# Performance work log

Hardware: AMD Instinct MI355X
Metric: run time of the kernel (lower is better)

The kernel has to match this reference:

```python
import jax, jax.numpy as jnp
import numpy as np

HIDDEN = 2048
NUM_HEADS = 16
HEAD_DIM = 128
INNER = NUM_HEADS * HEAD_DIM
ROPE_BASE = 10000.0


def apply_rope(x):
    # x: [B, H, S, D], rotate-half (NeoX-style) RoPE
    B, H, S, D = x.shape
    inv_freq = 1.0 / (ROPE_BASE ** (jnp.arange(0, D, 2, dtype=jnp.float32) / D))
    t = jnp.arange(S, dtype=jnp.float32)
    freqs = t[:, None] * inv_freq[None, :]          # [S, D/2]
    cos = jnp.concatenate([jnp.cos(freqs)] * 2, -1)  # [S, D]
    sin = jnp.concatenate([jnp.sin(freqs)] * 2, -1)
    x1, x2 = x[..., : D // 2], x[..., D // 2:]
    rotated = jnp.concatenate([-x2, x1], axis=-1)
    return x * cos[None, None] + rotated * sin[None, None]


def setup_inputs() -> dict:
    key = jax.random.key(0)
    ks = jax.random.split(key, 9)
    s = 1.0 / np.sqrt(HIDDEN)
    return {
        "hidden_states": jax.random.normal(ks[0], (2, 2048, HIDDEN), jnp.float32),
        "Wq": jax.random.uniform(ks[1], (INNER, HIDDEN), jnp.float32, -s, s),
        "bq": jax.random.uniform(ks[2], (INNER,), jnp.float32, -s, s),
        "Wk": jax.random.uniform(ks[3], (INNER, HIDDEN), jnp.float32, -s, s),
        "bk": jax.random.uniform(ks[4], (INNER,), jnp.float32, -s, s),
        "Wv": jax.random.uniform(ks[5], (INNER, HIDDEN), jnp.float32, -s, s),
        "bv": jax.random.uniform(ks[6], (INNER,), jnp.float32, -s, s),
        "Wo": jax.random.uniform(ks[7], (HIDDEN, INNER), jnp.float32, -s, s),
        "bo": jax.random.uniform(ks[8], (HIDDEN,), jnp.float32, -s, s),
    }


def reference(hidden_states, Wq, bq, Wk, bk, Wv, bv, Wo, bo):
    B, S, _ = hidden_states.shape

    def heads(x):  # [B,S,inner] -> [B,H,S,D]
        return x.reshape(B, S, NUM_HEADS, HEAD_DIM).transpose(0, 2, 1, 3)

    q = heads(hidden_states @ Wq.T + bq)
    k = heads(hidden_states @ Wk.T + bk)
    v = heads(hidden_states @ Wv.T + bv)
    q = apply_rope(q)
    k = apply_rope(k)

    scores = jnp.einsum("bhqd,bhkd->bhqk", q, k) / jnp.sqrt(
        jnp.asarray(HEAD_DIM, q.dtype))
    causal = jnp.tril(jnp.ones((S, S), dtype=bool))
    scores = jnp.where(causal[None, None], scores, jnp.finfo(scores.dtype).min)
    weights = jax.nn.softmax(scores, axis=-1)
    context = jnp.einsum("bhqk,bhkd->bhqd", weights, v)
    merged = context.transpose(0, 2, 1, 3).reshape(B, S, INNER)
    return merged @ Wo.T + bo
```

## Files before the change

### kernel.cpp

```cpp
#include <hip/hip_runtime.h>

using u16 = unsigned short;
using u32 = unsigned int;

typedef __attribute__((ext_vector_type(4))) float f32x4;
typedef __attribute__((ext_vector_type(8))) short frag8;

#define HIDDEN 2048
#define SEQ    2048
#define NHEADS 16
#define HDIM   128

__device__ __forceinline__ float bf2f(u16 u) {
  union { u32 i; float f; } c; c.i = ((u32)u) << 16; return c.f;
}
__device__ __forceinline__ u16 f2bf(float f) {
  union { float f; u32 i; } c; c.f = f;
  u32 u = c.i + 0x7fffu + ((c.i >> 16) & 1u);
  return (u16)(u >> 16);
}

__global__ void cvt_all(const float* __restrict__ X,
                        const float* __restrict__ W0, const float* __restrict__ W1,
                        const float* __restrict__ W2, const float* __restrict__ W3,
                        u16* __restrict__ dX,
                        u16* __restrict__ dW0, u16* __restrict__ dW1,
                        u16* __restrict__ dW2, u16* __restrict__ dW3)
{
  const int bx = blockIdx.x;
  const float* s; u16* d; int g;
  if (bx < 4096) { s = X; d = dX; g = bx * 256 + threadIdx.x; }
  else {
    const int t = bx - 4096;
    const int w = t >> 11;
    s = (w == 0) ? W0 : (w == 1) ? W1 : (w == 2) ? W2 : W3;
    d = (w == 0) ? dW0 : (w == 1) ? dW1 : (w == 2) ? dW2 : dW3;
    g = (t & 2047) * 256 + threadIdx.x;
  }
  const float* p = s + (size_t)g * 8;
  f32x4 x0 = *(const f32x4*)p, x1 = *(const f32x4*)(p + 4);
  frag8 o;
#pragma unroll
  for (int e = 0; e < 4; e++) { o[e] = (short)f2bf(x0[e]); o[e+4] = (short)f2bf(x1[e]); }
  *(frag8*)(d + (size_t)g * 8) = o;
}

template<int W_BF16, int NW, int VT, int C_F32>
__global__ __launch_bounds__(256, 4)
void gemm_fused(const u16* __restrict__ A,
                const void* __restrict__ W0, const void* __restrict__ W1,
                const void* __restrict__ W2,
                const float* __restrict__ bias0, const float* __restrict__ bias1,
                const float* __restrict__ bias2,
                void* __restrict__ C0, void* __restrict__ C1, void* __restrict__ C2)
{
  __shared__ __align__(16) u16 smem[8192];
  u16* As = smem;
  u16* Bs = smem + 4096;

  const int tid  = threadIdx.x;
  const int lane = tid & 63;
  const int wv   = tid >> 6;
  const int quad = lane >> 4;
  const int l16  = lane & 15;
  const int wm = wv >> 1, wn = wv & 1;
  const int m0 = blockIdx.y * 128;
  const int wix = (NW == 1) ? 0 : (blockIdx.x >> 4);
  const int n0  = ((NW == 1) ? blockIdx.x : (blockIdx.x & 15)) * 128;

  const void* Wp = (wix == 0) ? W0 : (wix == 1) ? W1 : W2;
  const float* bias = (wix == 0) ? bias0 : (wix == 1) ? bias1 : bias2;
  void* Cp = (wix == 0) ? C0 : (wix == 1) ? C1 : C2;

  f32x4 acc[4][4];
#pragma unroll
  for (int i = 0; i < 4; i++)
#pragma unroll
    for (int j = 0; j < 4; j++) acc[i][j] = (f32x4)0.0f;

  const int g0 = tid, g1 = tid + 256;
  const int r0 = g0 >> 2, c0 = (g0 & 3) * 8;
  const int r1 = g1 >> 2, c1 = (g1 & 3) * 8;

  for (int k0 = 0; k0 < HIDDEN; k0 += 32) {
    __builtin_amdgcn_global_load_lds(
      (const __attribute__((address_space(1))) void*)(A + (size_t)(m0 + r0) * HIDDEN + k0 + c0),
      (__attribute__((address_space(3))) void*)(As + g0 * 8), 16, 0, 0);
    __builtin_amdgcn_global_load_lds(
      (const __attribute__((address_space(1))) void*)(A + (size_t)(m0 + r1) * HIDDEN + k0 + c1),
      (__attribute__((address_space(3))) void*)(As + g1 * 8), 16, 0, 0);
    if (W_BF16) {
      const u16* Wb = (const u16*)Wp;
      __builtin_amdgcn_global_load_lds(
        (const __attribute__((address_space(1))) void*)(Wb + (size_t)(n0 + r0) * HIDDEN + k0 + c0),
        (__attribute__((address_space(3))) void*)(Bs + g0 * 8), 16, 0, 0);
      __builtin_amdgcn_global_load_lds(
        (const __attribute__((address_space(1))) void*)(Wb + (size_t)(n0 + r1) * HIDDEN + k0 + c1),
        (__attribute__((address_space(3))) void*)(Bs + g1 * 8), 16, 0, 0);
    } else {
      const float* Wf = (const float*)Wp;
      const float* p0 = Wf + (size_t)(n0 + r0) * HIDDEN + k0 + c0;
      const float* p1 = Wf + (size_t)(n0 + r1) * HIDDEN + k0 + c1;
      f32x4 x0 = *(const f32x4*)p0, x1 = *(const f32x4*)(p0 + 4);
      f32x4 y0 = *(const f32x4*)p1, y1 = *(const f32x4*)(p1 + 4);
      frag8 b0v, b1v;
#pragma unroll
      for (int e = 0; e < 4; e++) {
        b0v[e]   = (short)f2bf(x0[e]); b0v[e+4] = (short)f2bf(x1[e]);
        b1v[e]   = (short)f2bf(y0[e]); b1v[e+4] = (short)f2bf(y1[e]);
      }
      *(frag8*)&Bs[g0 * 8] = b0v;
      *(frag8*)&Bs[g1 * 8] = b1v;
    }

    __builtin_amdgcn_s_waitcnt(0);
    __syncthreads();

    frag8 af[4], bfr[4];
#pragma unroll
    for (int mt = 0; mt < 4; mt++)
      af[mt] = *(const frag8*)&As[(wm*64 + mt*16 + l16) * 32 + quad*8];
#pragma unroll
    for (int nt = 0; nt < 4; nt++)
      bfr[nt] = *(const frag8*)&Bs[(wn*64 + nt*16 + l16) * 32 + quad*8];
#pragma unroll
    for (int mt = 0; mt < 4; mt++)
#pragma unroll
      for (int nt = 0; nt < 4; nt++)
        acc[mt][nt] = __builtin_amdgcn_mfma_f32_16x16x32_bf16(af[mt], bfr[nt], acc[mt][nt], 0, 0, 0);

    __syncthreads();
  }

  if (VT && wix == 2) {
    u16* Cv = (u16*)Cp;
    u16* T = smem + wv * 1056;
#pragma unroll
    for (int nt = 0; nt < 4; nt++) {
      const int n  = n0 + wn*64 + nt*16 + l16;
      const float bv = bias[n];
#pragma unroll
      for (int mt = 0; mt < 4; mt++)
#pragma unroll
        for (int r = 0; r < 4; r++)
          T[l16 * 66 + mt*16 + quad*4 + r] = f2bf(acc[mt][nt][r] + bv);
#pragma unroll
      for (int rr = 0; rr < 16; rr++) {
        const int nn = n0 + wn*64 + nt*16 + rr;
        const int mm = m0 + wm*64 + lane;
        const int b = mm >> 11, s = mm & 2047;
        Cv[((size_t)(b * HIDDEN + nn)) * SEQ + s] = T[rr * 66 + lane];
      }
    }
  } else {
#pragma unroll
    for (int nt = 0; nt < 4; nt++) {
      const int n  = n0 + wn*64 + nt*16 + l16;
      const float bv = bias[n];
#pragma unroll
      for (int mt = 0; mt < 4; mt++) {
#pragma unroll
        for (int r = 0; r < 4; r++) {
          const int m = m0 + wm*64 + mt*16 + quad*4 + r;
          if (C_F32) ((float*)Cp)[(size_t)m * HIDDEN + n] = acc[mt][nt][r] + bv;
          else       ((u16*)Cp)[(size_t)m * HIDDEN + n]   = f2bf(acc[mt][nt][r] + bv);
        }
      }
    }
  }
}

#define NT32 32

#define STG(gptr, lofs) __builtin_amdgcn_global_load_lds( \
    (const __attribute__((address_space(1))) void*)(gptr), \
    (__attribute__((address_space(3))) void*)(smem + (lofs)), 16, 0, 0)

#define GRP(t, DOSTAGE, WAITSTR) { \
  u16* As = smem + ((t) % 3) * 24576; \
  u16* Bs = As + 16384; \
  frag8 af[8], bfr[2]; \
  _Pragma("unroll") for (int mt = 0; mt < 8; mt++) \
    af[mt] = *(const frag8*)(As + abase + mt*1024 + s0q); \
  bfr[0] = *(const frag8*)(Bs + bbase + s0q); \
  bfr[1] = *(const frag8*)(Bs + bbase + 1024 + s0q); \
  if (DOSTAGE) { \
    const size_t ko = (size_t)((t)+2)*64; const int sb = (((t)+2)%3)*24576; \
    STG(gA0 + ko, sb + ldsA0); STG(gA1 + ko, sb + ldsA1); STG(gB0 + ko, sb + ldsB0); \
  } \
  __builtin_amdgcn_s_barrier(); \
  __builtin_amdgcn_s_setprio(1); \
  _Pragma("unroll") for (int mt = 0; mt < 8; mt++) { \
    acc[mt][0] = __builtin_amdgcn_mfma_f32_16x16x32_bf16(af[mt], bfr[0], acc[mt][0], 0,0,0); \
    acc[mt][1] = __builtin_amdgcn_mfma_f32_16x16x32_bf16(af[mt], bfr[1], acc[mt][1], 0,0,0); \
  } \
  __builtin_amdgcn_s_setprio(0); \
  __builtin_amdgcn_s_barrier(); \
  _Pragma("unroll") for (int mt = 0; mt < 8; mt++) \
    af[mt] = *(const frag8*)(As + abase + mt*1024 + s1q); \
  bfr[0] = *(const frag8*)(Bs + bbase + s1q); \
  bfr[1] = *(const frag8*)(Bs + bbase + 1024 + s1q); \
  if (DOSTAGE) { \
    const size_t ko = (size_t)((t)+2)*64; const int sb = (((t)+2)%3)*24576; \
    STG(gA2 + ko, sb + ldsA2); STG(gA3 + ko, sb + ldsA3); STG(gB1 + ko, sb + ldsB1); \
  } \
  __builtin_amdgcn_s_barrier(); \
  __builtin_amdgcn_s_setprio(1); \
  _Pragma("unroll") for (int mt = 0; mt < 8; mt++) { \
    acc[mt][0] = __builtin_amdgcn_mfma_f32_16x16x32_bf16(af[mt], bfr[0], acc[mt][0], 0,0,0); \
    acc[mt][1] = __builtin_amdgcn_mfma_f32_16x16x32_bf16(af[mt], bfr[1], acc[mt][1], 0,0,0); \
  } \
  __builtin_amdgcn_s_setprio(0); \
  asm volatile("s_waitcnt " WAITSTR ::: "memory"); \
  __builtin_amdgcn_s_barrier(); \
}

#define G256_SETUP(Abase, Wbase) \
  const int tid  = threadIdx.x; \
  const int lane = tid & 63; \
  const int wv   = tid >> 6; \
  const int quad = lane >> 4; \
  const int l16  = lane & 15; \
  const int wm = wv >> 2, wn = wv & 3; \
  const int c8 = (lane & 7) ^ (lane >> 3); \
  const int rA = lane >> 3; \
  const u16* gA0 = (Abase) + (size_t)(m0 + wv*32 +  0 + rA) * HIDDEN + c8*8; \
  const u16* gA1 = (Abase) + (size_t)(m0 + wv*32 +  8 + rA) * HIDDEN + c8*8; \
  const u16* gA2 = (Abase) + (size_t)(m0 + wv*32 + 16 + rA) * HIDDEN + c8*8; \
  const u16* gA3 = (Abase) + (size_t)(m0 + wv*32 + 24 + rA) * HIDDEN + c8*8; \
  const u16* gB0 = (Wbase) + (size_t)(n0 + wv*16 +  0 + rA) * HIDDEN + c8*8; \
  const u16* gB1 = (Wbase) + (size_t)(n0 + wv*16 +  8 + rA) * HIDDEN + c8*8; \
  const int ldsA0 = (4*wv)*512 + lane*8; \
  const int ldsA1 = ldsA0 + 512; \
  const int ldsA2 = ldsA0 + 1024; \
  const int ldsA3 = ldsA0 + 1536; \
  const int ldsB0 = 16384 + (2*wv)*512 + lane*8; \
  const int ldsB1 = ldsB0 + 512; \
  const int s0q = ((quad    ) ^ (l16 & 7)) * 8; \
  const int s1q = ((quad + 4) ^ (l16 & 7)) * 8; \
  const int abase = (wm*128 + l16) * 64; \
  const int bbase = (wn*32  + l16) * 64; \
  f32x4 acc[8][2]; \
  _Pragma("unroll") \
  for (int i = 0; i < 8; i++) { acc[i][0] = (f32x4)0.0f; acc[i][1] = (f32x4)0.0f; } \
  STG(gA0, ldsA0); STG(gA1, ldsA1); STG(gB0, ldsB0); \
  STG(gA2, ldsA2); STG(gA3, ldsA3); STG(gB1, ldsB1); \
  STG(gA0 + 64, 24576 + ldsA0); STG(gA1 + 64, 24576 + ldsA1); STG(gB0 + 64, 24576 + ldsB0); \
  STG(gA2 + 64, 24576 + ldsA2); STG(gA3 + 64, 24576 + ldsA3); STG(gB1 + 64, 24576 + ldsB1); \
  asm volatile("s_waitcnt vmcnt(6)" ::: "memory"); \
  __builtin_amdgcn_s_barrier(); \
  for (int t = 0; t < NT32 - 2; ++t) GRP(t, 1, "vmcnt(6)"); \
  GRP(NT32 - 2, 0, "vmcnt(0)"); \
  GRP(NT32 - 1, 0, "vmcnt(63)");

__global__ __launch_bounds__(512, 2)
void gemm256_qkv(const u16* __restrict__ A,
                 const u16* __restrict__ W0, const u16* __restrict__ W1,
                 const u16* __restrict__ W2,
                 const float* __restrict__ bias0, const float* __restrict__ bias1,
                 const float* __restrict__ bias2,
                 u16* __restrict__ C0, u16* __restrict__ C1, u16* __restrict__ Vt)
{
  __shared__ __align__(16) u16 smem[73728];

  const int bid = blockIdx.x;
  const int sbid = (bid & 7) * 96 + (bid >> 3);
  const int colTile = sbid >> 4;
  const int rowTile = sbid & 15;
  const int wix = colTile >> 4;
  const int n0  = (colTile & 15) * 128;
  const int m0  = rowTile * 256;

  const u16* Wp = (wix == 0) ? W0 : (wix == 1) ? W1 : W2;
  const float* bias = (wix == 0) ? bias0 : (wix == 1) ? bias1 : bias2;

  G256_SETUP(A, Wp)

  if (wix != 2) {
    u16* Cb = (wix == 0) ? C0 : C1;
#pragma unroll
    for (int nt = 0; nt < 2; nt++) {
      const int n = n0 + wn*32 + nt*16 + l16;
      const float bv = bias[n];
#pragma unroll
      for (int mt = 0; mt < 8; mt++) {
        const int m = m0 + wm*128 + mt*16 + quad*4;
#pragma unroll
        for (int r = 0; r < 4; r++)
          Cb[(size_t)(m + r) * HIDDEN + n] = f2bf(acc[mt][nt][r] + bv);
      }
    }
  } else {
    u16* T = smem + wv * 2176;
    const int b  = m0 >> 11;
    const int s0 = (m0 & 2047) + wm*128;
#pragma unroll
    for (int nt = 0; nt < 2; nt++) {
      const int nloc = n0 + wn*32 + nt*16;
      const float bv = bias[nloc + l16];
#pragma unroll
      for (int mt = 0; mt < 8; mt++)
#pragma unroll
        for (int r = 0; r < 4; r++)
          T[l16*136 + mt*16 + quad*4 + r] = f2bf(acc[mt][nt][r] + bv);
#pragma unroll
      for (int rr = 0; rr < 16; rr++) {
        const size_t vb = ((size_t)(b * HIDDEN + nloc + rr)) * SEQ + s0;
        Vt[vb + lane]      = T[rr*136 + lane];
        Vt[vb + 64 + lane] = T[rr*136 + 64 + lane];
      }
    }
  }
}

__global__ __launch_bounds__(512, 2)
void gemm256_o(const u16* __restrict__ A, const u16* __restrict__ W,
               const float* __restrict__ bias, float* __restrict__ C)
{
  __shared__ __align__(16) u16 smem[73728];

  const int bid = blockIdx.x;
  const int sbid = (bid & 7) * 32 + (bid >> 3);
  const int colTile = sbid >> 4;
  const int rowTile = sbid & 15;
  const int n0  = colTile * 128;
  const int m0  = rowTile * 256;

  G256_SETUP(A, W)

#pragma unroll
  for (int nt = 0; nt < 2; nt++) {
    const int n = n0 + wn*32 + nt*16 + l16;
    const float bv = bias[n];
#pragma unroll
    for (int mt = 0; mt < 8; mt++) {
      const int m = m0 + wm*128 + mt*16 + quad*4;
#pragma unroll
      for (int r = 0; r < 4; r++)
        C[(size_t)(m + r) * HIDDEN + n] = acc[mt][nt][r] + bv;
    }
  }
}

__global__ void rope_kernel(u16* __restrict__ Q, u16* __restrict__ K)
{
  const int tid = blockIdx.x * 256 + threadIdx.x;
  const int t   = tid >> 19;
  const int r   = tid & 524287;
  const int row = r >> 7;
  const int grp = r & 127;
  const int h   = grp >> 3, d0 = (grp & 7) * 8;
  u16* X = t ? K : Q;
  const float s = (float)(row & 2047);
  const float qscale = t ? 1.0f : 0.08838834764831845f;
  const size_t base = (size_t)row * HIDDEN + h * HDIM + d0;
  frag8 a = *(const frag8*)(X + base);
  frag8 b = *(const frag8*)(X + base + 64);
  frag8 oa, ob;
#pragma unroll
  for (int e = 0; e < 8; e++) {
    const float inv = __expf(-(float)(d0 + e) * (9.210340371976184f / 64.0f));
    float sn, c;
    __sincosf(s * inv, &sn, &c);
    const float x1 = bf2f((u16)a[e]), x2 = bf2f((u16)b[e]);
    oa[e] = (short)f2bf((x1 * c - x2 * sn) * qscale);
    ob[e] = (short)f2bf((x2 * c + x1 * sn) * qscale);
  }
  *(frag8*)(X + base)      = oa;
  *(frag8*)(X + base + 64) = ob;
}

__global__ __launch_bounds__(256, 4)
void attn_kernel(const u16* Q, const u16* __restrict__ K,
                 const u16* __restrict__ Vt, u16* O)
{
  __shared__ __align__(16) u16 smem[20480];

  const int bx = blockIdx.x;
  const int g  = bx >> 5;
  const int bh = bx & 31;
  const int qt = (g & 1) ? (31 - (g >> 1)) : (g >> 1);
  const int b = bh >> 4, h = bh & 15;

  const int tid = threadIdx.x, lane = tid & 63, wv = tid >> 6;
  const int quad = lane >> 4, l16 = lane & 15;
  const int l7 = l16 & 7;

  const size_t krow0 = (size_t)(b * SEQ) * HIDDEN + h * HDIM;
  const size_t vrow0 = (size_t)(b * HIDDEN + h * HDIM) * SEQ;

  frag8 qf[4];
  const size_t qbase = ((size_t)(b * SEQ) + qt*64 + wv*16) * HIDDEN + h * HDIM;
#pragma unroll
  for (int ks = 0; ks < 4; ks++)
    qf[ks] = *(const frag8*)(Q + qbase + (size_t)l16 * HIDDEN + ks*32 + quad*8);

  const int kr4 = lane >> 4, kc = lane & 15;
  const int vr8 = lane >> 3;
  const u16* gK[4]; const u16* gV[4];
  int ldsK[4], ldsV[4];
#pragma unroll
  for (int it = 0; it < 4; it++) {
    const int kcs = kc ^ ((it*4 + kr4) & 7);
    gK[it] = K + krow0 + (size_t)(wv*16 + it*4 + kr4) * HIDDEN + kcs*8;
    ldsK[it] = (wv*16 + it*4)*128 + lane*8;
    const int vcs = (lane & 7) ^ vr8;
    gV[it] = Vt + vrow0 + (size_t)(wv*32 + it*8 + vr8) * SEQ + vcs*8;
    ldsV[it] = 8192 + (wv*32 + it*8)*64 + lane*8;
  }

  f32x4 Oacc[8];
#pragma unroll
  for (int dt = 0; dt < 8; dt++) Oacc[dt] = (f32x4)0.0f;
  float m_i[4], l_i[4];
#pragma unroll
  for (int r = 0; r < 4; r++) { m_i[r] = -1e30f; l_i[r] = 0.0f; }

  const int ktmax = qt + 1;
  u16* Pw = smem + 16384 + wv*1024;

  for (int kt = 0; kt < ktmax; kt++) {
#pragma unroll
    for (int it = 0; it < 4; it++) {
      __builtin_amdgcn_global_load_lds(
        (const __attribute__((address_space(1))) void*)(gK[it] + (size_t)kt*64*HIDDEN),
        (__attribute__((address_space(3))) void*)(smem + ldsK[it]), 16, 0, 0);
      __builtin_amdgcn_global_load_lds(
        (const __attribute__((address_space(1))) void*)(gV[it] + kt*64),
        (__attribute__((address_space(3))) void*)(smem + ldsV[it]), 16, 0, 0);
    }
    asm volatile("s_waitcnt vmcnt(0)" ::: "memory");
    __syncthreads();

    f32x4 st[4];
#pragma unroll
    for (int jt = 0; jt < 4; jt++) st[jt] = (f32x4)0.0f;

    __builtin_amdgcn_s_setprio(1);
#pragma unroll
    for (int ks = 0; ks < 4; ks++) {
      frag8 kf[4];
#pragma unroll
      for (int jt = 0; jt < 4; jt++)
        kf[jt] = *(const frag8*)&smem[(jt*16 + l16)*128 + ((ks*4 + quad) ^ l7)*8];
#pragma unroll
      for (int jt = 0; jt < 4; jt++)
        st[jt] = __builtin_amdgcn_mfma_f32_16x16x32_bf16(qf[ks], kf[jt], st[jt], 0, 0, 0);
    }
    __builtin_amdgcn_s_setprio(0);

    if (kt == qt) {
#pragma unroll
      for (int jt = 0; jt < 4; jt++) {
        const int jl = jt*16 + l16;
#pragma unroll
        for (int r = 0; r < 4; r++) {
          const int ml = wv*16 + quad*4 + r;
          st[jt][r] = (jl <= ml) ? st[jt][r] : -1e30f;
        }
      }
    }

    float alpha[4];
    int needresc = 0;
#pragma unroll
    for (int r = 0; r < 4; r++) {
      float cm = fmaxf(fmaxf(st[0][r], st[1][r]), fmaxf(st[2][r], st[3][r]));
      cm = fmaxf(cm, __shfl_xor(cm, 1, 64));
      cm = fmaxf(cm, __shfl_xor(cm, 2, 64));
      cm = fmaxf(cm, __shfl_xor(cm, 4, 64));
      cm = fmaxf(cm, __shfl_xor(cm, 8, 64));
      if (cm > m_i[r] + 8.0f) {
        alpha[r] = __expf(m_i[r] - cm);
        m_i[r] = cm;
        needresc = 1;
      } else {
        alpha[r] = 1.0f;
      }
    }

    float csum[4];
#pragma unroll
    for (int r = 0; r < 4; r++) csum[r] = 0.0f;
#pragma unroll
    for (int jt = 0; jt < 4; jt++)
#pragma unroll
      for (int r = 0; r < 4; r++) {
        const float p = __expf(st[jt][r] - m_i[r]);
        csum[r] += p;
        const int prow = quad*4 + r;
        Pw[prow*64 + (((jt*2 + (l16 >> 3)) ^ (prow & 7)) << 3) + l7] = f2bf(p);
      }
#pragma unroll
    for (int r = 0; r < 4; r++) {
      float cs = csum[r];
      cs += __shfl_xor(cs, 1, 64);
      cs += __shfl_xor(cs, 2, 64);
      cs += __shfl_xor(cs, 4, 64);
      cs += __shfl_xor(cs, 8, 64);
      l_i[r] = l_i[r] * alpha[r] + cs;
    }
    if (__any(needresc)) {
#pragma unroll
      for (int r = 0; r < 4; r++)
#pragma unroll
        for (int dt = 0; dt < 8; dt++) Oacc[dt][r] *= alpha[r];
    }

    __builtin_amdgcn_s_setprio(1);
#pragma unroll
    for (int ks2 = 0; ks2 < 2; ks2++) {
      frag8 pf = *(const frag8*)&Pw[l16*64 + ((ks2*4 + quad) ^ l7)*8];
#pragma unroll
      for (int dt = 0; dt < 8; dt++) {
        frag8 vf = *(const frag8*)&smem[8192 + (dt*16 + l16)*64 + ((ks2*4 + quad) ^ l7)*8];
        Oacc[dt] = __builtin_amdgcn_mfma_f32_16x16x32_bf16(pf, vf, Oacc[dt], 0, 0, 0);
      }
    }
    __builtin_amdgcn_s_setprio(0);
    __syncthreads();
  }

#pragma unroll
  for (int r = 0; r < 4; r++) {
    const float inv = 1.0f / l_i[r];
    const int m = qt*64 + wv*16 + quad*4 + r;
#pragma unroll
    for (int dt = 0; dt < 8; dt++) {
      const int d = dt*16 + l16;
      O[((size_t)(b * SEQ) + m) * HIDDEN + h * HDIM + d] = f2bf(Oacc[dt][r] * inv);
    }
  }
}

extern "C" void kernel_launch(void* const* d_in, const int* in_sizes, int n_in,
                              void* d_out, int out_size, void* d_ws, size_t ws_size,
                              hipStream_t stream)
{
  const float* X  = (const float*)d_in[0];
  const float* Wq = (const float*)d_in[1];
  const float* bq = (const float*)d_in[2];
  const float* Wk = (const float*)d_in[3];
  const float* bk = (const float*)d_in[4];
  const float* Wv = (const float*)d_in[5];
  const float* bv = (const float*)d_in[6];
  const float* Wo = (const float*)d_in[7];
  const float* bo = (const float*)d_in[8];
  float* out = (float*)d_out;

  u16* Kb = (u16*)d_out;
  u16* Xb = (u16*)d_out + (8u << 20);
  char* ws = (char*)d_ws;
  u16* Qb  = (u16*)ws;
  u16* Vtb = (u16*)(ws + (16u << 20));

  dim3 blk(256);
  const bool fast = ws_size >= (64u << 20);
  if (fast) {
    u16* Wqb = (u16*)(ws + (32u << 20));
    u16* Wkb = (u16*)(ws + (40u << 20));
    u16* Wvb = (u16*)(ws + (48u << 20));
    u16* Wob = (u16*)(ws + (56u << 20));
    cvt_all<<<12288, blk, 0, stream>>>(X, Wq, Wk, Wv, Wo, Xb, Wqb, Wkb, Wvb, Wob);
    gemm256_qkv<<<dim3(768), dim3(512), 0, stream>>>(
        Xb, Wqb, Wkb, Wvb, bq, bk, bv, Qb, Kb, Vtb);
    rope_kernel<<<4096, blk, 0, stream>>>(Qb, Kb);
    attn_kernel<<<1024, blk, 0, stream>>>(Qb, Kb, Vtb, Qb);
    gemm256_o<<<dim3(256), dim3(512), 0, stream>>>(Qb, Wob, bo, out);
  } else {
    cvt_all<<<4096, blk, 0, stream>>>(X, Wq, Wk, Wv, Wo, Xb, Xb, Xb, Xb, Xb);
    gemm_fused<0,3,1,0><<<dim3(48,32), blk, 0, stream>>>(
        Xb, Wq, Wk, Wv, bq, bk, bv, Qb, Kb, Vtb);
    rope_kernel<<<4096, blk, 0, stream>>>(Qb, Kb);
    attn_kernel<<<1024, blk, 0, stream>>>(Qb, Kb, Vtb, Qb);
    gemm_fused<0,1,0,1><<<dim3(16,32), blk, 0, stream>>>(
        Qb, Wo, Wo, Wo, bo, bo, bo, out, out, out);
  }
}
```

Before: 444.3 us.

## Fuse RoPE into QKV GEMM epilogue and reshape warp tiling to 4x4

Moves RoPE and the query scaling into the QKV GEMM epilogue. The accumulator tile is staged through shared memory so each thread holds both halves of a head dimension, and the output is written as 16-byte vectors. This removes the separate rope kernel and its extra read/write pass over Q and K. The warp layout changes from 2x4 warps each covering 128x32 to 4x2 warps each covering 64x64, which lowers LDS fragment loads per MFMA. The attention kernel's launch-bounds occupancy hint also drops from 4 to 3, which may change register allocation.

After: 408.0 us. 1.09x faster.

```diff
diff --git a/kernel.cpp b/kernel.cpp
--- a/kernel.cpp
+++ b/kernel.cpp
@@ -179,37 +179,35 @@
 #define GRP(t, DOSTAGE, WAITSTR) { \
   u16* As = smem + ((t) % 3) * 24576; \
   u16* Bs = As + 16384; \
-  frag8 af[8], bfr[2]; \
-  _Pragma("unroll") for (int mt = 0; mt < 8; mt++) \
+  frag8 af[4], bfr[4]; \
+  _Pragma("unroll") for (int mt = 0; mt < 4; mt++) \
     af[mt] = *(const frag8*)(As + abase + mt*1024 + s0q); \
-  bfr[0] = *(const frag8*)(Bs + bbase + s0q); \
-  bfr[1] = *(const frag8*)(Bs + bbase + 1024 + s0q); \
+  _Pragma("unroll") for (int nt = 0; nt < 4; nt++) \
+    bfr[nt] = *(const frag8*)(Bs + bbase + nt*1024 + s0q); \
   if (DOSTAGE) { \
     const size_t ko = (size_t)((t)+2)*64; const int sb = (((t)+2)%3)*24576; \
     STG(gA0 + ko, sb + ldsA0); STG(gA1 + ko, sb + ldsA1); STG(gB0 + ko, sb + ldsB0); \
   } \
   __builtin_amdgcn_s_barrier(); \
   __builtin_amdgcn_s_setprio(1); \
-  _Pragma("unroll") for (int mt = 0; mt < 8; mt++) { \
-    acc[mt][0] = __builtin_amdgcn_mfma_f32_16x16x32_bf16(af[mt], bfr[0], acc[mt][0], 0,0,0); \
-    acc[mt][1] = __builtin_amdgcn_mfma_f32_16x16x32_bf16(af[mt], bfr[1], acc[mt][1], 0,0,0); \
-  } \
+  _Pragma("unroll") for (int mt = 0; mt < 4; mt++) \
+    _Pragma("unroll") for (int nt = 0; nt < 4; nt++) \
+      acc[mt][nt] = __builtin_amdgcn_mfma_f32_16x16x32_bf16(af[mt], bfr[nt], acc[mt][nt], 0,0,0); \
   __builtin_amdgcn_s_setprio(0); \
   __builtin_amdgcn_s_barrier(); \
-  _Pragma("unroll") for (int mt = 0; mt < 8; mt++) \
+  _Pragma("unroll") for (int mt = 0; mt < 4; mt++) \
     af[mt] = *(const frag8*)(As + abase + mt*1024 + s1q); \
-  bfr[0] = *(const frag8*)(Bs + bbase + s1q); \
-  bfr[1] = *(const frag8*)(Bs + bbase + 1024 + s1q); \
+  _Pragma("unroll") for (int nt = 0; nt < 4; nt++) \
+    bfr[nt] = *(const frag8*)(Bs + bbase + nt*1024 + s1q); \
   if (DOSTAGE) { \
     const size_t ko = (size_t)((t)+2)*64; const int sb = (((t)+2)%3)*24576; \
     STG(gA2 + ko, sb + ldsA2); STG(gA3 + ko, sb + ldsA3); STG(gB1 + ko, sb + ldsB1); \
   } \
   __builtin_amdgcn_s_barrier(); \
   __builtin_amdgcn_s_setprio(1); \
-  _Pragma("unroll") for (int mt = 0; mt < 8; mt++) { \
-    acc[mt][0] = __builtin_amdgcn_mfma_f32_16x16x32_bf16(af[mt], bfr[0], acc[mt][0], 0,0,0); \
-    acc[mt][1] = __builtin_amdgcn_mfma_f32_16x16x32_bf16(af[mt], bfr[1], acc[mt][1], 0,0,0); \
-  } \
+  _Pragma("unroll") for (int mt = 0; mt < 4; mt++) \
+    _Pragma("unroll") for (int nt = 0; nt < 4; nt++) \
+      acc[mt][nt] = __builtin_amdgcn_mfma_f32_16x16x32_bf16(af[mt], bfr[nt], acc[mt][nt], 0,0,0); \
   __builtin_amdgcn_s_setprio(0); \
   asm volatile("s_waitcnt " WAITSTR ::: "memory"); \
   __builtin_amdgcn_s_barrier(); \
@@ -221,7 +219,7 @@
   const int wv   = tid >> 6; \
   const int quad = lane >> 4; \
   const int l16  = lane & 15; \
-  const int wm = wv >> 2, wn = wv & 3; \
+  const int wm = wv >> 1, wn = wv & 1; \
   const int c8 = (lane & 7) ^ (lane >> 3); \
   const int rA = lane >> 3; \
   const u16* gA0 = (Abase) + (size_t)(m0 + wv*32 +  0 + rA) * HIDDEN + c8*8; \
@@ -238,11 +236,13 @@
   const int ldsB1 = ldsB0 + 512; \
   const int s0q = ((quad    ) ^ (l16 & 7)) * 8; \
   const int s1q = ((quad + 4) ^ (l16 & 7)) * 8; \
-  const int abase = (wm*128 + l16) * 64; \
-  const int bbase = (wn*32  + l16) * 64; \
-  f32x4 acc[8][2]; \
+  const int abase = (wm*64 + l16) * 64; \
+  const int bbase = (wn*64 + l16) * 64; \
+  f32x4 acc[4][4]; \
   _Pragma("unroll") \
-  for (int i = 0; i < 8; i++) { acc[i][0] = (f32x4)0.0f; acc[i][1] = (f32x4)0.0f; } \
+  for (int i = 0; i < 4; i++) \
+    _Pragma("unroll") \
+    for (int j = 0; j < 4; j++) acc[i][j] = (f32x4)0.0f; \
   STG(gA0, ldsA0); STG(gA1, ldsA1); STG(gB0, ldsB0); \
   STG(gA2, ldsA2); STG(gA3, ldsA3); STG(gB1, ldsB1); \
   STG(gA0 + 64, 24576 + ldsA0); STG(gA1 + 64, 24576 + ldsA1); STG(gB0 + 64, 24576 + ldsB0); \
@@ -277,37 +277,60 @@
   G256_SETUP(A, Wp)
 
   if (wix != 2) {
+    const float scale = (wix == 0) ? 0.08838834764831845f : 1.0f;
+    u16* T = smem;
+#pragma unroll
+    for (int nt = 0; nt < 4; nt++) {
+      const int nl = wn*64 + nt*16 + l16;
+      const float bv = bias[n0 + nl];
+#pragma unroll
+      for (int mt = 0; mt < 4; mt++) {
+        const int ml = wm*64 + mt*16 + quad*4;
+#pragma unroll
+        for (int r = 0; r < 4; r++)
+          T[(ml + r)*128 + nl] = f2bf((acc[mt][nt][r] + bv) * scale);
+      }
+    }
+    __syncthreads();
+
     u16* Cb = (wix == 0) ? C0 : C1;
-#pragma unroll
-    for (int nt = 0; nt < 2; nt++) {
-      const int n = n0 + wn*32 + nt*16 + l16;
-      const float bv = bias[n];
-#pragma unroll
-      for (int mt = 0; mt < 8; mt++) {
-        const int m = m0 + wm*128 + mt*16 + quad*4;
+    const int mr = tid >> 1, qd = tid & 1;
+    const float s = (float)((m0 + mr) & 2047);
+#pragma unroll
+    for (int c8i = 0; c8i < 4; c8i++) {
+      const int d0 = qd*32 + c8i*8;
+      frag8 lo = *(const frag8*)&T[mr*128 + d0];
+      frag8 hi = *(const frag8*)&T[mr*128 + 64 + d0];
+      frag8 olo, ohi;
+#pragma unroll
+      for (int e = 0; e < 8; e++) {
+        const float inv = __expf(-(float)(d0 + e) * (9.210340371976184f / 64.0f));
+        float sn, c;
+        __sincosf(s * inv, &sn, &c);
+        const float x1 = bf2f((u16)lo[e]), x2 = bf2f((u16)hi[e]);
+        olo[e] = (short)f2bf(x1 * c - x2 * sn);
+        ohi[e] = (short)f2bf(x2 * c + x1 * sn);
+      }
+      *(frag8*)&Cb[(size_t)(m0 + mr) * HIDDEN + n0 + d0]      = olo;
+      *(frag8*)&Cb[(size_t)(m0 + mr) * HIDDEN + n0 + 64 + d0] = ohi;
+    }
+  } else {
+    u16* T = smem + wv * 1152;
+    const int b  = m0 >> 11;
+    const int s0 = (m0 & 2047) + wm*64;
+#pragma unroll
+    for (int nt = 0; nt < 4; nt++) {
+      const int nloc = n0 + wn*64 + nt*16;
+      const float bv = bias[nloc + l16];
+#pragma unroll
+      for (int mt = 0; mt < 4; mt++)
 #pragma unroll
         for (int r = 0; r < 4; r++)
-          Cb[(size_t)(m + r) * HIDDEN + n] = f2bf(acc[mt][nt][r] + bv);
-      }
-    }
-  } else {
-    u16* T = smem + wv * 2176;
-    const int b  = m0 >> 11;
-    const int s0 = (m0 & 2047) + wm*128;
-#pragma unroll
-    for (int nt = 0; nt < 2; nt++) {
-      const int nloc = n0 + wn*32 + nt*16;
-      const float bv = bias[nloc + l16];
-#pragma unroll
-      for (int mt = 0; mt < 8; mt++)
-#pragma unroll
-        for (int r = 0; r < 4; r++)
-          T[l16*136 + mt*16 + quad*4 + r] = f2bf(acc[mt][nt][r] + bv);
+          T[l16*72 + mt*16 + quad*4 + r] = f2bf(acc[mt][nt][r] + bv);
 #pragma unroll
       for (int rr = 0; rr < 16; rr++) {
         const size_t vb = ((size_t)(b * HIDDEN + nloc + rr)) * SEQ + s0;
-        Vt[vb + lane]      = T[rr*136 + lane];
-        Vt[vb + 64 + lane] = T[rr*136 + 64 + lane];
+        Vt[vb + lane] = T[rr*72 + lane];
       }
     }
   }
@@ -329,12 +352,12 @@
   G256_SETUP(A, W)
 
 #pragma unroll
-  for (int nt = 0; nt < 2; nt++) {
-    const int n = n0 + wn*32 + nt*16 + l16;
+  for (int nt = 0; nt < 4; nt++) {
+    const int n = n0 + wn*64 + nt*16 + l16;
     const float bv = bias[n];
 #pragma unroll
-    for (int mt = 0; mt < 8; mt++) {
-      const int m = m0 + wm*128 + mt*16 + quad*4;
+    for (int mt = 0; mt < 4; mt++) {
+      const int m = m0 + wm*64 + mt*16 + quad*4;
 #pragma unroll
       for (int r = 0; r < 4; r++)
         C[(size_t)(m + r) * HIDDEN + n] = acc[mt][nt][r] + bv;
@@ -370,7 +393,7 @@
   *(frag8*)(X + base + 64) = ob;
 }
 
-__global__ __launch_bounds__(256, 4)
+__global__ __launch_bounds__(256, 3)
 void attn_kernel(const u16* Q, const u16* __restrict__ K,
                  const u16* __restrict__ Vt, u16* O)
 {
@@ -564,7 +587,6 @@
     cvt_all<<<12288, blk, 0, stream>>>(X, Wq, Wk, Wv, Wo, Xb, Wqb, Wkb, Wvb, Wob);
     gemm256_qkv<<<dim3(768), dim3(512), 0, stream>>>(
         Xb, Wqb, Wkb, Wvb, bq, bk, bv, Qb, Kb, Vtb);
-    rope_kernel<<<4096, blk, 0, stream>>>(Qb, Kb);
     attn_kernel<<<1024, blk, 0, stream>>>(Qb, Kb, Vtb, Qb);
     gemm256_o<<<dim3(256), dim3(512), 0, stream>>>(Qb, Wob, bo, out);
   } else {
```
